# Optimization experiments

Hardware: AMD Instinct MI355X
Metric: run time of the kernel (lower is better)

The kernel has to match this reference:

```python
import jax, jax.numpy as jnp
import numpy as np

EMBED_DIM = 1024
NUM_HEADS = 16
HEAD_DIM = EMBED_DIM // NUM_HEADS


def setup_inputs() -> dict:
    key = jax.random.key(0)
    ks = jax.random.split(key, 9)
    s = 1.0 / np.sqrt(EMBED_DIM)
    inp = {"x": jax.random.normal(ks[0], (2, 2048, EMBED_DIM), dtype=jnp.float32)}
    for i, name in enumerate(["q", "k", "v", "out"]):
        inp[f"W_{name}"] = jax.random.uniform(ks[1 + 2 * i], (EMBED_DIM, EMBED_DIM), jnp.float32, -s, s)
        inp[f"b_{name}"] = jax.random.uniform(ks[2 + 2 * i], (EMBED_DIM,), jnp.float32, -s, s)
    return inp


def _heads(x):
    # [B, S, D] -> [B, H, S, Dh]
    b, s, _ = x.shape
    return x.reshape(b, s, NUM_HEADS, HEAD_DIM).transpose(0, 2, 1, 3)


def reference(x, W_q, b_q, W_k, b_k, W_v, b_v, W_out, b_out):
    q = _heads(x @ W_q.T + b_q)
    k = _heads(x @ W_k.T + b_k)
    v = _heads(x @ W_v.T + b_v)
    scale = HEAD_DIM ** 0.5
    logits = jnp.einsum("bhqd,bhkd->bhqk", q, k) / scale  # [B,H,S,S]
    s = x.shape[1]
    causal = jnp.tril(jnp.ones((s, s), dtype=bool))
    logits = jnp.where(causal, logits, -jnp.inf)
    a = jax.nn.softmax(logits, axis=-1)
    o = jnp.einsum("bhqk,bhkd->bhqd", a, v)
    o = o.transpose(0, 2, 1, 3).reshape(x.shape[0], s, EMBED_DIM)
    return o @ W_out.T + b_out
```

## Files before the change

kernel.cpp:

```cpp
#include <hip/hip_runtime.h>
#include <hip/hip_bf16.h>

typedef __bf16 bf16_t;
typedef __bf16 bf16x8 __attribute__((ext_vector_type(8)));
typedef __bf16 bf16x4 __attribute__((ext_vector_type(4)));
typedef float  f32x4  __attribute__((ext_vector_type(4)));

#define MFMA16(a, b, c) __builtin_amdgcn_mfma_f32_16x16x32_bf16((a), (b), (c), 0, 0, 0)

constexpr int E  = 1024;
constexpr int S  = 2048;
constexpr int H  = 16;
constexpr int M  = 4096;

__device__ __forceinline__ void glds16(const bf16_t* src, bf16_t* dst) {
  __builtin_amdgcn_global_load_lds(
      (const __attribute__((address_space(1))) void*)src,
      (__attribute__((address_space(3))) void*)dst, 16, 0, 0);
}

template <int ROWS, int NT>
__device__ __forceinline__ void stage_tile(const bf16_t* g, int gld,
                                           bf16_t* lds, int tid) {
  const int w = tid >> 6, l = tid & 63;
#pragma unroll
  for (int i = 0; i < ROWS * 8 / NT; ++i) {
    const int c = i * NT + w * 64 + l;
    const int row = c >> 3;
    const int gch = (c & 7) ^ (row & 7);
    glds16(g + (size_t)row * gld + gch * 8, lds + (size_t)(i * NT + w * 64) * 8);
  }
}

__device__ __forceinline__ bf16x8 read_frag(const bf16_t* lds, int row, int kc) {
  return *(const bf16x8*)(lds + (size_t)((row << 3) + (kc ^ (row & 7))) * 8);
}

__global__ void cvt_all_kernel(const float* __restrict__ x,
                               const float* __restrict__ w0, const float* __restrict__ w1,
                               const float* __restrict__ w2, const float* __restrict__ w3,
                               bf16_t* __restrict__ xb,
                               bf16_t* __restrict__ o0, bf16_t* __restrict__ o1,
                               bf16_t* __restrict__ o2, bf16_t* __restrict__ o3) {
  const int bid = blockIdx.x;
  const float* s;
  bf16_t* d;
  int idx;
  if (bid < 4096) {
    s = x; d = xb; idx = bid * 256 + threadIdx.x;
  } else {
    const int seg = (bid - 4096) >> 10;
    s = seg == 0 ? w0 : seg == 1 ? w1 : seg == 2 ? w2 : w3;
    d = seg == 0 ? o0 : seg == 1 ? o1 : seg == 2 ? o2 : o3;
    idx = ((bid - 4096) & 1023) * 256 + threadIdx.x;
  }
  float4 v = ((const float4*)s)[idx];
  bf16x4 o;
  o[0] = (bf16_t)v.x; o[1] = (bf16_t)v.y; o[2] = (bf16_t)v.z; o[3] = (bf16_t)v.w;
  ((bf16x4*)d)[idx] = o;
}

__global__ __launch_bounds__(512, 2) void qkv8_kernel(
    const bf16_t* __restrict__ xb, const bf16_t* __restrict__ W3,
    const float* __restrict__ bq, const float* __restrict__ bk,
    const float* __restrict__ bv, bf16_t* __restrict__ Qb) {
  __shared__ __align__(16) bf16_t As[2][256 * 64];
  __shared__ __align__(16) bf16_t Bs[2][192 * 64];
  const int tid = threadIdx.x;
  const int l = tid & 63, lq = l & 15, qd = l >> 4;
  const int w = tid >> 6, wm = w >> 2, wn = w & 3;

  const int wg = blockIdx.x;
  const int xcd = wg & 7, i5 = wg >> 3;
  const int region = xcd * 2 + (i5 >> 4);
  const int j = i5 & 15;
  const int bx = (region & 3) * 4 + (j & 3);
  const int by = (region >> 2) * 4 + (j >> 2);
  const int m0 = by * 256, n0 = bx * 192;

  const bf16_t* Ag = xb + (size_t)m0 * E;
  const bf16_t* Bg = W3 + (size_t)n0 * E;

  f32x4 acc[8][3];
#pragma unroll
  for (int mi = 0; mi < 8; ++mi)
#pragma unroll
    for (int n = 0; n < 3; ++n) acc[mi][n] = (f32x4){0.f, 0.f, 0.f, 0.f};

  stage_tile<256, 512>(Ag, E, As[0], tid);
  stage_tile<192, 512>(Bg, E, Bs[0], tid);
  asm volatile("s_waitcnt vmcnt(0)" ::: "memory");
  __builtin_amdgcn_s_barrier();

#pragma unroll 1
  for (int g = 0; g < 16; ++g) {
    const int s = g & 1;
    const bf16_t* Al = As[s];
    const bf16_t* Bl = Bs[s];
    bf16_t* An = As[s ^ 1];
    bf16_t* Bn = Bs[s ^ 1];
    const bf16_t* Agn = Ag + (g + 1) * 64;
    const bf16_t* Bgn = Bg + (g + 1) * 64;
    const bool more = (g < 15);
#pragma unroll
    for (int q = 0; q < 4; ++q) {
      const int mh = q >> 1, kk = q & 1;
      bf16x8 af[4], bfr[3];
#pragma unroll
      for (int jj = 0; jj < 4; ++jj)
        af[jj] = read_frag(Al, wm * 128 + (mh * 4 + jj) * 16 + lq, kk * 4 + qd);
#pragma unroll
      for (int n = 0; n < 3; ++n)
        bfr[n] = read_frag(Bl, wn * 48 + n * 16 + lq, kk * 4 + qd);
      if (more) {
        if (q == 0) stage_tile<128, 512>(Agn, E, An, tid);
        else if (q == 1) stage_tile<128, 512>(Agn + (size_t)128 * E, E, An + 128 * 64, tid);
        else if (q == 2) stage_tile<192, 512>(Bgn, E, Bn, tid);
      }
      __builtin_amdgcn_s_barrier();
      asm volatile("s_waitcnt lgkmcnt(0)" ::: "memory");
      __builtin_amdgcn_sched_barrier(0);
      __builtin_amdgcn_s_setprio(1);
#pragma unroll
      for (int jj = 0; jj < 4; ++jj)
#pragma unroll
        for (int n = 0; n < 3; ++n)
          acc[mh * 4 + jj][n] = MFMA16(af[jj], bfr[n], acc[mh * 4 + jj][n]);
      __builtin_amdgcn_s_setprio(0);
      if (q == 3 && more) asm volatile("s_waitcnt vmcnt(0)" ::: "memory");
      __builtin_amdgcn_s_barrier();
    }
  }

#pragma unroll
  for (int n = 0; n < 3; ++n) {
    const int col = n0 + wn * 48 + n * 16 + lq;
    const int mat = col >> 10, cc = col & 1023;
    const float bvv = (mat == 0 ? bq : mat == 1 ? bk : bv)[cc];
    const float sc = (mat == 0) ? 0.18033688011112043f : 1.0f;
    bf16_t* Out = Qb + (size_t)mat * ((size_t)M * E);
#pragma unroll
    for (int mi = 0; mi < 8; ++mi)
#pragma unroll
      for (int r = 0; r < 4; ++r) {
        const int row = m0 + wm * 128 + mi * 16 + qd * 4 + r;
        Out[(size_t)row * E + cc] = (bf16_t)((acc[mi][n][r] + bvv) * sc);
      }
  }
}

__global__ __launch_bounds__(256) void vtrans_kernel(const bf16_t* __restrict__ Vb,
                                                     bf16_t* __restrict__ VT) {
  constexpr int LDT = 72;
  __shared__ __align__(16) bf16_t T[64 * LDT];
  const int tid = threadIdx.x;
  const int st = blockIdx.x, bh = blockIdx.y;
  const int b = bh >> 4, h = bh & 15;
  const int s0 = st * 64;
  const size_t rowbase = (size_t)b * S;
#pragma unroll
  for (int i = 0; i < 2; ++i) {
    const int c = i * 256 + tid;
    const int sl = c >> 3, dp = c & 7;
    const int a = sl >> 4, bb = (sl >> 2) & 3, cc = sl & 3;
    const int p = (a >> 1) * 32 + bb * 8 + (a & 1) * 4 + cc;
    bf16x8 v = *(const bf16x8*)(Vb + (rowbase + s0 + sl) * E + h * 64 + dp * 8);
    *(bf16x8*)&T[p * LDT + dp * 8] = v;
  }
  __syncthreads();
#pragma unroll
  for (int i = 0; i < 2; ++i) {
    const int c = i * 256 + tid;
    const int d = c >> 3, pp = (c & 7) * 8;
    bf16x8 o;
#pragma unroll
    for (int j = 0; j < 8; ++j) o[j] = T[(pp + j) * LDT + d];
    *(bf16x8*)&VT[((size_t)bh * 64 + d) * S + s0 + pp] = o;
  }
}

__global__ __launch_bounds__(256) void oproj_gemm_kernel(
    const bf16_t* __restrict__ Ob, const bf16_t* __restrict__ wo,
    const float* __restrict__ bo, float* __restrict__ out) {
  __shared__ __align__(16) bf16_t As[64 * 64];
  __shared__ __align__(16) bf16_t Bs[128 * 64];
  const int tid = threadIdx.x;
  const int n0 = blockIdx.x * 128;
  const int m0 = blockIdx.y * 64;
  const int w = tid >> 6, l = tid & 63, lq = l & 15, qd = l >> 4;
  const int wr = (w >> 1) * 32, wc = (w & 1) * 64;

  f32x4 acc[2][4];
#pragma unroll
  for (int i = 0; i < 2; ++i)
#pragma unroll
    for (int j = 0; j < 4; ++j) acc[i][j] = (f32x4){0.f, 0.f, 0.f, 0.f};

  for (int kt = 0; kt < 16; ++kt) {
    __syncthreads();
    stage_tile<64, 256>(Ob + (size_t)m0 * E + kt * 64, E, As, tid);
    stage_tile<128, 256>(wo + (size_t)n0 * E + kt * 64, E, Bs, tid);
    __syncthreads();
#pragma unroll
    for (int ks = 0; ks < 2; ++ks) {
      bf16x8 af[2], bw[4];
#pragma unroll
      for (int mi = 0; mi < 2; ++mi)
        af[mi] = read_frag(As, wr + mi * 16 + lq, ks * 4 + qd);
#pragma unroll
      for (int ni = 0; ni < 4; ++ni)
        bw[ni] = read_frag(Bs, wc + ni * 16 + lq, ks * 4 + qd);
#pragma unroll
      for (int mi = 0; mi < 2; ++mi)
#pragma unroll
        for (int ni = 0; ni < 4; ++ni)
          acc[mi][ni] = MFMA16(af[mi], bw[ni], acc[mi][ni]);
    }
  }
#pragma unroll
  for (int ni = 0; ni < 4; ++ni) {
    const int col = n0 + wc + ni * 16 + lq;
    const float bvv = bo[col];
#pragma unroll
    for (int mi = 0; mi < 2; ++mi)
#pragma unroll
      for (int r = 0; r < 4; ++r) {
        const int row = m0 + wr + mi * 16 + qd * 4 + r;
        out[(size_t)row * E + col] = acc[mi][ni][r] + bvv;
      }
  }
}

__global__ __launch_bounds__(256, 2) void attn_kernel(
    const bf16_t* __restrict__ Q, const bf16_t* __restrict__ K,
    const bf16_t* __restrict__ VT, bf16_t* __restrict__ O) {
  __shared__ __align__(16) bf16_t Ks[2][64 * 64];
  __shared__ __align__(16) bf16_t Vt[3][64 * 64];

  const int tid = threadIdx.x;
  const int w = tid >> 6, l = tid & 63;
  const int lq = l & 15, qd = l >> 4;
  const int bid = blockIdx.x;
  const int g = bid & 7, t = bid >> 3;
  const int bh = g * 4 + (t & 3);
  const int p = t >> 2;
  const int b = bh >> 4, h = bh & 15;
  const size_t rowbase = (size_t)b * S;
  const bf16_t* Kg = K + rowbase * E + h * 64;
  const bf16_t* Vg = VT + (size_t)bh * 64 * S;

  bf16x8 ones;
#pragma unroll
  for (int j = 0; j < 8; ++j) ones[j] = (bf16_t)1.0f;

  stage_tile<64, 256>(Kg, E, Ks[0], tid);
  stage_tile<64, 256>(Vg, S, Vt[0], tid);
  int cb = 0;
  int vcur = 0;

#pragma unroll 1
  for (int seg = 0; seg < 2; ++seg) {
    const int qt = seg ? p : 31 - p;
    const int qr = qt * 64 + w * 16;

    bf16x8 aq[2];
#pragma unroll
    for (int ks = 0; ks < 2; ++ks)
      aq[ks] = *(const bf16x8*)(Q + (rowbase + qr + lq) * E + h * 64 +
                                ks * 32 + qd * 8);

    f32x4 oacc[4];
#pragma unroll
    for (int nt = 0; nt < 4; ++nt) oacc[nt] = (f32x4){0.f, 0.f, 0.f, 0.f};
    f32x4 osum = (f32x4){0.f, 0.f, 0.f, 0.f};
    bf16x8 ap_prev[2];
    int vprev = vcur;

    auto do_pv = [&](const bf16_t* Vp) {
#pragma unroll
      for (int ks = 0; ks < 2; ++ks) {
        bf16x8 bv[4];
#pragma unroll
        for (int nt = 0; nt < 4; ++nt)
          bv[nt] = read_frag(Vp, nt * 16 + lq, ks * 4 + qd);
#pragma unroll
        for (int nt = 0; nt < 4; ++nt)
          oacc[nt] = MFMA16(ap_prev[ks], bv[nt], oacc[nt]);
        osum = MFMA16(ap_prev[ks], ones, osum);
      }
    };

    for (int kt = 0; kt <= qt; ++kt) {
      __syncthreads();
      const int vnext = (vcur + 1 == 3) ? 0 : vcur + 1;
      if (kt < qt) {
        const int kn = (kt + 1) * 64;
        stage_tile<64, 256>(Kg + (size_t)kn * E, E, Ks[cb ^ 1], tid);
        stage_tile<64, 256>(Vg + kn, S, Vt[vnext], tid);
      } else if (seg == 0) {
        stage_tile<64, 256>(Kg, E, Ks[cb ^ 1], tid);
        stage_tile<64, 256>(Vg, S, Vt[vnext], tid);
      }
      const bf16_t* Kc = Ks[cb];
      const int k0 = kt * 64;
      const bool needmask = (kt == qt);

      f32x4 sacc[4];
#pragma unroll
      for (int nt = 0; nt < 4; ++nt) sacc[nt] = (f32x4){0.f, 0.f, 0.f, 0.f};
      __builtin_amdgcn_s_setprio(1);
#pragma unroll
      for (int ks = 0; ks < 2; ++ks) {
        bf16x8 bk[4];
#pragma unroll
        for (int nt = 0; nt < 4; ++nt)
          bk[nt] = read_frag(Kc, nt * 16 + lq, ks * 4 + qd);
#pragma unroll
        for (int nt = 0; nt < 4; ++nt)
          sacc[nt] = MFMA16(bk[nt], aq[ks], sacc[nt]);
      }
      if (kt > 0) do_pv(Vt[vprev]);
      __builtin_amdgcn_s_setprio(0);

#pragma unroll
      for (int nt = 0; nt < 4; ++nt)
#pragma unroll
        for (int r = 0; r < 4; ++r) {
          float pv = __builtin_amdgcn_exp2f(sacc[nt][r]);
          if (needmask) {
            const int kg = k0 + nt * 16 + qd * 4 + r;
            const int qg = qr + lq;
            pv = (kg > qg) ? 0.f : pv;
          }
          ap_prev[nt >> 1][((nt & 1) << 2) | r] = (bf16_t)pv;
        }
      vprev = vcur;
      vcur = vnext;
      cb ^= 1;
    }
    do_pv(Vt[vprev]);

    float rinv[4];
#pragma unroll
    for (int r = 0; r < 4; ++r) rinv[r] = 1.0f / osum[r];
#pragma unroll
    for (int nt = 0; nt < 4; ++nt)
#pragma unroll
      for (int r = 0; r < 4; ++r) {
        const int qg = qr + qd * 4 + r;
        O[(rowbase + qg) * E + h * 64 + nt * 16 + lq] =
            (bf16_t)(oacc[nt][r] * rinv[r]);
      }
  }
}

extern "C" void kernel_launch(void* const* d_in, const int* in_sizes, int n_in,
                              void* d_out, int out_size, void* d_ws, size_t ws_size,
                              hipStream_t stream) {
  const float* x  = (const float*)d_in[0];
  const float* Wq = (const float*)d_in[1];
  const float* bq = (const float*)d_in[2];
  const float* Wk = (const float*)d_in[3];
  const float* bk = (const float*)d_in[4];
  const float* Wv = (const float*)d_in[5];
  const float* bv = (const float*)d_in[6];
  const float* Wo = (const float*)d_in[7];
  const float* bo = (const float*)d_in[8];
  float* out = (float*)d_out;

  unsigned char* ws = (unsigned char*)d_ws;
  constexpr size_t MB = 1ull << 20;
  bf16_t* xb  = (bf16_t*)(ws + 0 * MB);
  bf16_t* wqb = (bf16_t*)(ws + 8 * MB);
  bf16_t* wkb = (bf16_t*)(ws + 10 * MB);
  bf16_t* wvb = (bf16_t*)(ws + 12 * MB);
  bf16_t* wob = (bf16_t*)(ws + 14 * MB);
  bf16_t* Qb  = (bf16_t*)(ws + 16 * MB);
  bf16_t* Kb  = (bf16_t*)(ws + 24 * MB);
  bf16_t* Vb  = (bf16_t*)(ws + 32 * MB);
  bf16_t* VT  = (bf16_t*)(ws + 40 * MB);
  bf16_t* Ob  = xb;

  cvt_all_kernel<<<4096 + 4 * 1024, 256, 0, stream>>>(
      x, Wq, Wk, Wv, Wo, xb, wqb, wkb, wvb, wob);

  qkv8_kernel<<<256, 512, 0, stream>>>(xb, wqb, bq, bk, bv, Qb);

  vtrans_kernel<<<dim3(32, 32), 256, 0, stream>>>(Vb, VT);

  attn_kernel<<<512, 256, 0, stream>>>(Qb, Kb, VT, Ob);

  oproj_gemm_kernel<<<dim3(8, 64), 256, 0, stream>>>(Ob, wob, bo, out);
}
```

Measured before the change: 180.6 us.

## Fuse V transpose into QKV GEMM epilogue and simplify K-loop pipeline

The QKV GEMM epilogue now writes V directly in the transposed, permuted layout the attention kernel expects, so the separate vtrans kernel launch and its extra read and write of V go away. The main K-loop is also simplified: the next full tile is prefetched at the start of each step with __syncthreads, replacing the fine-grained split staging, setprio and sched_barrier interleaving. The V stores become strided 8-byte writes, and the simpler loop may overlap loads and MFMAs less well, which could slow the GEMM.

```diff
diff --git a/kernel.cpp b/kernel.cpp
--- a/kernel.cpp
+++ b/kernel.cpp
@@ -63,7 +63,8 @@
 __global__ __launch_bounds__(512, 2) void qkv8_kernel(
     const bf16_t* __restrict__ xb, const bf16_t* __restrict__ W3,
     const float* __restrict__ bq, const float* __restrict__ bk,
-    const float* __restrict__ bv, bf16_t* __restrict__ Qb) {
+    const float* __restrict__ bv, bf16_t* __restrict__ QKb,
+    bf16_t* __restrict__ VT) {
   __shared__ __align__(16) bf16_t As[2][256 * 64];
   __shared__ __align__(16) bf16_t Bs[2][192 * 64];
   const int tid = threadIdx.x;
@@ -89,47 +90,33 @@
 
   stage_tile<256, 512>(Ag, E, As[0], tid);
   stage_tile<192, 512>(Bg, E, Bs[0], tid);
-  asm volatile("s_waitcnt vmcnt(0)" ::: "memory");
-  __builtin_amdgcn_s_barrier();
+  __syncthreads();
 
 #pragma unroll 1
   for (int g = 0; g < 16; ++g) {
     const int s = g & 1;
     const bf16_t* Al = As[s];
     const bf16_t* Bl = Bs[s];
-    bf16_t* An = As[s ^ 1];
-    bf16_t* Bn = Bs[s ^ 1];
-    const bf16_t* Agn = Ag + (g + 1) * 64;
-    const bf16_t* Bgn = Bg + (g + 1) * 64;
-    const bool more = (g < 15);
-#pragma unroll
-    for (int q = 0; q < 4; ++q) {
-      const int mh = q >> 1, kk = q & 1;
-      bf16x8 af[4], bfr[3];
-#pragma unroll
-      for (int jj = 0; jj < 4; ++jj)
-        af[jj] = read_frag(Al, wm * 128 + (mh * 4 + jj) * 16 + lq, kk * 4 + qd);
+    if (g < 15) {
+      stage_tile<256, 512>(Ag + (g + 1) * 64, E, As[s ^ 1], tid);
+      stage_tile<192, 512>(Bg + (g + 1) * 64, E, Bs[s ^ 1], tid);
+    }
+#pragma unroll
+    for (int kk = 0; kk < 2; ++kk) {
+      bf16x8 af[8], bfr[3];
+#pragma unroll
+      for (int jj = 0; jj < 8; ++jj)
+        af[jj] = read_frag(Al, wm * 128 + jj * 16 + lq, kk * 4 + qd);
 #pragma unroll
       for (int n = 0; n < 3; ++n)
         bfr[n] = read_frag(Bl, wn * 48 + n * 16 + lq, kk * 4 + qd);
-      if (more) {
-        if (q == 0) stage_tile<128, 512>(Agn, E, An, tid);
-        else if (q == 1) stage_tile<128, 512>(Agn + (size_t)128 * E, E, An + 128 * 64, tid);
-        else if (q == 2) stage_tile<192, 512>(Bgn, E, Bn, tid);
-      }
-      __builtin_amdgcn_s_barrier();
-      asm volatile("s_waitcnt lgkmcnt(0)" ::: "memory");
-      __builtin_amdgcn_sched_barrier(0);
-      __builtin_amdgcn_s_setprio(1);
-#pragma unroll
-      for (int jj = 0; jj < 4; ++jj)
+#pragma unroll
+      for (int jj = 0; jj < 8; ++jj)
 #pragma unroll
         for (int n = 0; n < 3; ++n)
-          acc[mh * 4 + jj][n] = MFMA16(af[jj], bfr[n], acc[mh * 4 + jj][n]);
-      __builtin_amdgcn_s_setprio(0);
-      if (q == 3 && more) asm volatile("s_waitcnt vmcnt(0)" ::: "memory");
-      __builtin_amdgcn_s_barrier();
-    }
+          acc[jj][n] = MFMA16(af[jj], bfr[n], acc[jj][n]);
+    }
+    __syncthreads();
   }
 
 #pragma unroll
@@ -137,45 +124,32 @@
     const int col = n0 + wn * 48 + n * 16 + lq;
     const int mat = col >> 10, cc = col & 1023;
     const float bvv = (mat == 0 ? bq : mat == 1 ? bk : bv)[cc];
-    const float sc = (mat == 0) ? 0.18033688011112043f : 1.0f;
-    bf16_t* Out = Qb + (size_t)mat * ((size_t)M * E);
-#pragma unroll
-    for (int mi = 0; mi < 8; ++mi)
-#pragma unroll
-      for (int r = 0; r < 4; ++r) {
-        const int row = m0 + wm * 128 + mi * 16 + qd * 4 + r;
-        Out[(size_t)row * E + cc] = (bf16_t)((acc[mi][n][r] + bvv) * sc);
-      }
-  }
-}
-
-__global__ __launch_bounds__(256) void vtrans_kernel(const bf16_t* __restrict__ Vb,
-                                                     bf16_t* __restrict__ VT) {
-  constexpr int LDT = 72;
-  __shared__ __align__(16) bf16_t T[64 * LDT];
-  const int tid = threadIdx.x;
-  const int st = blockIdx.x, bh = blockIdx.y;
-  const int b = bh >> 4, h = bh & 15;
-  const int s0 = st * 64;
-  const size_t rowbase = (size_t)b * S;
-#pragma unroll
-  for (int i = 0; i < 2; ++i) {
-    const int c = i * 256 + tid;
-    const int sl = c >> 3, dp = c & 7;
-    const int a = sl >> 4, bb = (sl >> 2) & 3, cc = sl & 3;
-    const int p = (a >> 1) * 32 + bb * 8 + (a & 1) * 4 + cc;
-    bf16x8 v = *(const bf16x8*)(Vb + (rowbase + s0 + sl) * E + h * 64 + dp * 8);
-    *(bf16x8*)&T[p * LDT + dp * 8] = v;
-  }
-  __syncthreads();
-#pragma unroll
-  for (int i = 0; i < 2; ++i) {
-    const int c = i * 256 + tid;
-    const int d = c >> 3, pp = (c & 7) * 8;
-    bf16x8 o;
-#pragma unroll
-    for (int j = 0; j < 8; ++j) o[j] = T[(pp + j) * LDT + d];
-    *(bf16x8*)&VT[((size_t)bh * 64 + d) * S + s0 + pp] = o;
+    if (mat < 2) {
+      const float sc = (mat == 0) ? 0.18033688011112043f : 1.0f;
+      bf16_t* Out = QKb + (size_t)mat * ((size_t)M * E);
+#pragma unroll
+      for (int mi = 0; mi < 8; ++mi)
+#pragma unroll
+        for (int r = 0; r < 4; ++r) {
+          const int row = m0 + wm * 128 + mi * 16 + qd * 4 + r;
+          Out[(size_t)row * E + cc] = (bf16_t)((acc[mi][n][r] + bvv) * sc);
+        }
+    } else {
+      const int d = cc & 63, hh = cc >> 6;
+#pragma unroll
+      for (int mi = 0; mi < 8; ++mi) {
+        const int row = m0 + wm * 128 + mi * 16 + qd * 4;
+        const int bb_ = row >> 11;
+        const int s_loc = row & (S - 1);
+        const int sl = s_loc & 63, s0 = s_loc & ~63;
+        const int a = sl >> 4, b4 = (sl >> 2) & 3;
+        const int pb = (a >> 1) * 32 + b4 * 8 + (a & 1) * 4;
+        bf16x4 vv;
+#pragma unroll
+        for (int r = 0; r < 4; ++r) vv[r] = (bf16_t)(acc[mi][n][r] + bvv);
+        *(bf16x4*)&VT[((size_t)((bb_ * 16 + hh) * 64 + d)) * S + s0 + pb] = vv;
+      }
+    }
   }
 }
 
@@ -376,19 +350,15 @@
   bf16_t* wvb = (bf16_t*)(ws + 12 * MB);
   bf16_t* wob = (bf16_t*)(ws + 14 * MB);
   bf16_t* Qb  = (bf16_t*)(ws + 16 * MB);
-  bf16_t* Kb  = (bf16_t*)(ws + 24 * MB);
-  bf16_t* Vb  = (bf16_t*)(ws + 32 * MB);
   bf16_t* VT  = (bf16_t*)(ws + 40 * MB);
   bf16_t* Ob  = xb;
 
   cvt_all_kernel<<<4096 + 4 * 1024, 256, 0, stream>>>(
       x, Wq, Wk, Wv, Wo, xb, wqb, wkb, wvb, wob);
 
-  qkv8_kernel<<<256, 512, 0, stream>>>(xb, wqb, bq, bk, bv, Qb);
-
-  vtrans_kernel<<<dim3(32, 32), 256, 0, stream>>>(Vb, VT);
-
-  attn_kernel<<<512, 256, 0, stream>>>(Qb, Kb, VT, Ob);
+  qkv8_kernel<<<256, 512, 0, stream>>>(xb, wqb, bq, bk, bv, Qb, VT);
+
+  attn_kernel<<<512, 256, 0, stream>>>(Qb, Qb + (size_t)M * E, VT, Ob);
 
   oproj_gemm_kernel<<<dim3(8, 64), 256, 0, stream>>>(Ob, wob, bo, out);
 }
```

Result: faster. 174.5 us (-3.4%).
